# Optimization experiments

Hardware: AMD Instinct MI355X
Metric: run time of the kernel (lower is better)

The kernel has to match this reference:

```python
import jax, jax.numpy as jnp
import numpy as np
import math

# Static multi-level spatial layout (H, W) per level and flattened start offsets.
SHAPES = ((100, 100), (50, 50), (25, 25), (13, 13))
STARTS = (0, 10000, 12500, 13125)
LEN_IN = 13294
D_MODEL, N_LEVELS, N_HEADS, N_POINTS = 256, 4, 8, 4
D_HEAD = D_MODEL // N_HEADS
B, LQ = 2, 13294


def _offset_bias():
    # Replicates MSDeformAttn._reset_parameters radial grid init for sampling_offsets.bias
    thetas = np.arange(N_HEADS, dtype=np.float32) * (2.0 * math.pi / N_HEADS)
    grid = np.stack([np.cos(thetas), np.sin(thetas)], axis=-1)  # [nh, 2]
    grid = grid / np.abs(grid).max(axis=-1, keepdims=True)
    # [nh, nl, np, 2] with per-point radius (i+1)
    full = np.tile(grid[:, None, None, :], (1, N_LEVELS, N_POINTS, 1))
    full = full * np.arange(1, N_POINTS + 1, dtype=np.float32)[None, None, :, None]
    return full.reshape(-1)


def setup_inputs() -> dict:
    key = jax.random.key(0)
    ks = jax.random.split(key, 8)
    xavier = 1.0 / math.sqrt(D_MODEL)
    return {
        "query": jax.random.normal(ks[0], (B, LQ, D_MODEL), jnp.float32),
        "reference_points": jax.random.uniform(ks[1], (B, LQ, N_LEVELS, 2), jnp.float32),
        "input_flatten": jax.random.normal(ks[2], (B, LEN_IN, D_MODEL), jnp.float32),
        "input_spatial_shapes": jnp.array(SHAPES, jnp.int32),
        "input_level_start_index": jnp.array(STARTS, jnp.int32),
        "W_off": jax.random.normal(ks[3], (D_MODEL, N_HEADS * N_LEVELS * N_POINTS * 2), jnp.float32) * 0.01,
        "b_off": jnp.asarray(_offset_bias()),
        "W_attn": jax.random.normal(ks[4], (D_MODEL, N_HEADS * N_LEVELS * N_POINTS), jnp.float32) * 0.02,
        "b_attn": jnp.zeros((N_HEADS * N_LEVELS * N_POINTS,), jnp.float32),
        "W_val": jax.random.normal(ks[5], (D_MODEL, D_MODEL), jnp.float32) * xavier,
        "b_val": jnp.zeros((D_MODEL,), jnp.float32),
        "W_out": jax.random.normal(ks[6], (D_MODEL, D_MODEL), jnp.float32) * xavier,
        "b_out": jnp.zeros((D_MODEL,), jnp.float32),
    }


def reference(query, reference_points, input_flatten, input_spatial_shapes,
              input_level_start_index, W_off, b_off, W_attn, b_attn,
              W_val, b_val, W_out, b_out):
    Bq, Lq, _ = query.shape
    value = (input_flatten @ W_val + b_val).reshape(Bq, LEN_IN, N_HEADS, D_HEAD)

    off = (query @ W_off + b_off).reshape(Bq, Lq, N_HEADS, N_LEVELS, N_POINTS, 2)
    aw = (query @ W_attn + b_attn).reshape(Bq, Lq, N_HEADS, N_LEVELS * N_POINTS)
    aw = jax.nn.softmax(aw, axis=-1).reshape(Bq, Lq, N_HEADS, N_LEVELS, N_POINTS)

    # offset normalizer is (W, H) per level
    normalizer = jnp.array([[w, h] for (h, w) in SHAPES], query.dtype)  # [nl, 2]
    loc = reference_points[:, :, None, :, None, :] + off / normalizer[None, None, None, :, None, :]

    bi = jnp.arange(Bq)[:, None, None, None]
    hi = jnp.arange(N_HEADS)[None, None, :, None]
    out = jnp.zeros((Bq, Lq, N_HEADS, D_HEAD), query.dtype)

    # Per-level zero-padded bilinear sampling (math-equivalent to grid_sample
    # align_corners=False, padding_mode='zeros' on the padded max_H x max_W grid,
    # since the padded region is zero-filled).
    for lvl, (H, W) in enumerate(SHAPES):
        s = STARTS[lvl]
        vflat = value[:, s:s + H * W]  # [B, H*W, nh, dh]
        l = loc[:, :, :, lvl]          # [B, Lq, nh, P, 2] in normalized coords
        x = l[..., 0] * W - 0.5
        y = l[..., 1] * H - 0.5
        x0 = jnp.floor(x)
        y0 = jnp.floor(y)
        sampled = jnp.zeros((Bq, Lq, N_HEADS, N_POINTS, D_HEAD), query.dtype)
        for dx in (0, 1):
            for dy in (0, 1):
                xi = x0 + dx
                yi = y0 + dy
                wgt = (1.0 - jnp.abs(x - xi)) * (1.0 - jnp.abs(y - yi))
                valid = (xi >= 0) & (xi <= W - 1) & (yi >= 0) & (yi <= H - 1)
                idx = (jnp.clip(yi, 0, H - 1) * W + jnp.clip(xi, 0, W - 1)).astype(jnp.int32)
                v = vflat[bi, idx, hi]  # [B, Lq, nh, P, dh]
                sampled = sampled + v * (wgt * valid)[..., None]
        out = out + jnp.einsum('bqhpd,bqhp->bqhd', sampled, aw[:, :, :, lvl])

    out = out.reshape(Bq, Lq, D_MODEL)
    return out @ W_out + b_out
```

## Files before the change

### kernel.cpp

```cpp
#include <hip/hip_runtime.h>
#include <math.h>

#define BQ 2
#define LQ 13294
#define LEN_IN 13294
#define M_ROWS 26588

__device__ __constant__ int c_HW[4]    = {100, 50, 25, 13};
__device__ __constant__ int c_START[4] = {0, 10000, 12500, 13125};

typedef __attribute__((ext_vector_type(8))) short bf16x8;
typedef __attribute__((ext_vector_type(4))) float f32x4;
typedef __attribute__((ext_vector_type(2))) float f32x2;

__device__ inline unsigned short f2bf(float f) {
  union { float f; unsigned int u; } x; x.f = f;
  unsigned int u = x.u;
  return (unsigned short)((u + 0x7fffu + ((u >> 16) & 1u)) >> 16);
}
__device__ inline float h2f(unsigned short h) {
  _Float16 x; __builtin_memcpy(&x, &h, 2); return (float)x;
}
__device__ inline unsigned short f2h(float f) {
  _Float16 x = (_Float16)f; unsigned short u; __builtin_memcpy(&u, &x, 2); return u;
}

__device__ inline void gl_lds16(const void* g, void* l) {
  __builtin_amdgcn_global_load_lds(
      (const __attribute__((address_space(1))) unsigned int*)g,
      (__attribute__((address_space(3))) unsigned int*)l, 16, 0, 0);
}

__global__ __launch_bounds__(256) void prep_w(
    const float* __restrict__ W_off, const float* __restrict__ b_off,
    const float* __restrict__ W_attn, const float* __restrict__ b_attn,
    const float* __restrict__ W_val, const float* __restrict__ W_out,
    unsigned short* __restrict__ Wval_t, unsigned short* __restrict__ Woa_t,
    unsigned short* __restrict__ Wout_t, float* __restrict__ b_oa) {
  const int idx = blockIdx.x * 256 + threadIdx.x;
  const int SZ1 = 256 * 256;
  const int SZ2 = 384 * 256;
  if (idx < SZ1) {
    const int n = idx >> 8, k = idx & 255;
    Wval_t[idx] = f2bf(W_val[k * 256 + n]);
  } else if (idx < SZ1 + SZ2) {
    const int j = idx - SZ1;
    const int n = j >> 8, k = j & 255;
    const float v = (n < 256) ? W_off[k * 256 + n] : W_attn[k * 128 + (n - 256)];
    Woa_t[j] = f2bf(v);
  } else {
    const int j = idx - SZ1 - SZ2;
    const int n = j >> 8, k = j & 255;
    Wout_t[j] = f2bf(W_out[k * 256 + n]);
  }
  if (blockIdx.x == 0) b_oa[threadIdx.x] = b_off[threadIdx.x];
  if (blockIdx.x == 1 && threadIdx.x < 128)
    b_oa[256 + threadIdx.x] = b_attn[threadIdx.x];
}

__device__ inline void stage_W(const unsigned short* __restrict__ Wt,
                               int n0, int wv, int lane, unsigned short* Ws) {
#pragma unroll
  for (int it = 0; it < 16; ++it) {
    const int lin = wv * 1024 + it * 64 + lane;
    const int r = lin >> 5;
    const int p = lin & 31;
    const int c = p ^ (r & 7);
    gl_lds16(Wt + (size_t)(n0 + r) * 256 + c * 8,
             &Ws[(size_t)(wv * 1024 + it * 64) * 8]);
  }
}

template <int CT>
__device__ inline void kloop_epilogue(
    const bf16x8* a0f, const bf16x8* a1f, const unsigned short* Ws,
    const float* __restrict__ bias, void* __restrict__ Cp,
    int M, int N, int m0, int n0, int wv, int fr, int fq) {
  f32x4 acc[2][8];
#pragma unroll
  for (int mt = 0; mt < 2; ++mt)
#pragma unroll
    for (int n = 0; n < 8; ++n) acc[mt][n] = (f32x4){0.f, 0.f, 0.f, 0.f};

#pragma unroll
  for (int kk = 0; kk < 8; ++kk) {
#pragma unroll
    for (int n = 0; n < 8; ++n) {
      const int rn = n * 16 + fr;
      const bf16x8 b =
          *(const bf16x8*)&Ws[rn * 256 + (((kk * 4 + fq) ^ (rn & 7)) * 8)];
      acc[0][n] = __builtin_amdgcn_mfma_f32_16x16x32_bf16(b, a0f[kk], acc[0][n], 0, 0, 0);
      acc[1][n] = __builtin_amdgcn_mfma_f32_16x16x32_bf16(b, a1f[kk], acc[1][n], 0, 0, 0);
    }
  }

#pragma unroll
  for (int n = 0; n < 8; ++n) {
    const int nb = n0 + n * 16 + fq * 4;
    const float4 b4 = *(const float4*)&bias[nb];
#pragma unroll
    for (int mt = 0; mt < 2; ++mt) {
      const int m = m0 + wv * 32 + mt * 16 + fr;
      if (m >= M) continue;
      const float v0 = acc[mt][n][0] + b4.x;
      const float v1 = acc[mt][n][1] + b4.y;
      const float v2 = acc[mt][n][2] + b4.z;
      const float v3 = acc[mt][n][3] + b4.w;
      if (CT == 0) {
        *(float4*)&((float*)Cp)[(size_t)m * N + nb] = make_float4(v0, v1, v2, v3);
      } else if (CT == 1) {
        uint2 o;
        o.x = (unsigned int)f2bf(v0) | ((unsigned int)f2bf(v1) << 16);
        o.y = (unsigned int)f2bf(v2) | ((unsigned int)f2bf(v3) << 16);
        *(uint2*)&((unsigned short*)Cp)[(size_t)m * N + nb] = o;
      } else {
        uint2 o;
        o.x = (unsigned int)f2h(v0) | ((unsigned int)f2h(v1) << 16);
        o.y = (unsigned int)f2h(v2) | ((unsigned int)f2h(v3) << 16);
        *(uint2*)&((unsigned short*)Cp)[(size_t)m * N + nb] = o;
      }
    }
  }
}

template <int CT>
__device__ inline void gemm_stream_f32A(
    const float* __restrict__ A, const unsigned short* __restrict__ Wt,
    const float* __restrict__ bias, void* __restrict__ Cp,
    int M, int N, int m0, int n0, unsigned short* Ws) {
  const int tid = threadIdx.x;
  const int wv = tid >> 6;
  const int lane = tid & 63;
  const int fr = lane & 15;
  const int fq = lane >> 4;

  int mr0 = m0 + wv * 32 + fr;       if (mr0 > M - 1) mr0 = M - 1;
  int mr1 = m0 + wv * 32 + 16 + fr;  if (mr1 > M - 1) mr1 = M - 1;
  const float* a0 = A + (size_t)mr0 * 256 + fq * 8;
  const float* a1 = A + (size_t)mr1 * 256 + fq * 8;

  bf16x8 a0f[8], a1f[8];
#pragma unroll
  for (int kk = 0; kk < 8; ++kk) {
    const float4 x0 = *(const float4*)(a0 + kk * 32);
    const float4 x1 = *(const float4*)(a0 + kk * 32 + 4);
    const float4 y0 = *(const float4*)(a1 + kk * 32);
    const float4 y1 = *(const float4*)(a1 + kk * 32 + 4);
    ushort4 h0, h1;
    h0.x = f2bf(x0.x); h0.y = f2bf(x0.y); h0.z = f2bf(x0.z); h0.w = f2bf(x0.w);
    h1.x = f2bf(x1.x); h1.y = f2bf(x1.y); h1.z = f2bf(x1.z); h1.w = f2bf(x1.w);
    union { ushort4 h[2]; bf16x8 v; } u0; u0.h[0] = h0; u0.h[1] = h1;
    a0f[kk] = u0.v;
    h0.x = f2bf(y0.x); h0.y = f2bf(y0.y); h0.z = f2bf(y0.z); h0.w = f2bf(y0.w);
    h1.x = f2bf(y1.x); h1.y = f2bf(y1.y); h1.z = f2bf(y1.z); h1.w = f2bf(y1.w);
    union { ushort4 h[2]; bf16x8 v; } u1; u1.h[0] = h0; u1.h[1] = h1;
    a1f[kk] = u1.v;
  }

  stage_W(Wt, n0, wv, lane, Ws);
  __syncthreads();

  kloop_epilogue<CT>(a0f, a1f, Ws, bias, Cp, M, N, m0, n0, wv, fr, fq);
}

template <int CT>
__device__ inline void gemm_stream_bf16A(
    const unsigned short* __restrict__ A, const unsigned short* __restrict__ Wt,
    const float* __restrict__ bias, void* __restrict__ Cp,
    int M, int N, int m0, int n0, unsigned short* Ws) {
  const int tid = threadIdx.x;
  const int wv = tid >> 6;
  const int lane = tid & 63;
  const int fr = lane & 15;
  const int fq = lane >> 4;

  int mr0 = m0 + wv * 32 + fr;       if (mr0 > M - 1) mr0 = M - 1;
  int mr1 = m0 + wv * 32 + 16 + fr;  if (mr1 > M - 1) mr1 = M - 1;
  const unsigned short* a0 = A + (size_t)mr0 * 256 + fq * 8;
  const unsigned short* a1 = A + (size_t)mr1 * 256 + fq * 8;
  bf16x8 a0f[8], a1f[8];
#pragma unroll
  for (int kk = 0; kk < 8; ++kk) {
    a0f[kk] = *(const bf16x8*)(a0 + kk * 32);
    a1f[kk] = *(const bf16x8*)(a1 + kk * 32);
  }

  stage_W(Wt, n0, wv, lane, Ws);
  __syncthreads();

  kloop_epilogue<CT>(a0f, a1f, Ws, bias, Cp, M, N, m0, n0, wv, fr, fq);
}

__global__ __launch_bounds__(256) void gemm_vo(
    const float* __restrict__ inpf, const float* __restrict__ query,
    const unsigned short* __restrict__ Wval_t,
    const unsigned short* __restrict__ Woa_t,
    const float* __restrict__ b_val, const float* __restrict__ b_oa,
    void* __restrict__ v_buf, void* __restrict__ oa_buf) {
  __shared__ unsigned short Ws[128 * 256];
  const int m0 = blockIdx.x * 128;
  if (blockIdx.y < 2) {
    gemm_stream_f32A<1>(inpf, Wval_t, b_val, v_buf, M_ROWS, 256,
                        m0, blockIdx.y * 128, Ws);
  } else {
    gemm_stream_f32A<2>(query, Woa_t, b_oa, oa_buf, M_ROWS, 384,
                        m0, (blockIdx.y - 2) * 128, Ws);
  }
}

__global__ __launch_bounds__(256) void gemm_out(
    const unsigned short* __restrict__ mid,
    const unsigned short* __restrict__ Wout_t,
    const float* __restrict__ b_out, float* __restrict__ out) {
  __shared__ unsigned short Ws[128 * 256];
  gemm_stream_bf16A<0>(mid, Wout_t, b_out, out, M_ROWS, 256,
                       blockIdx.x * 128, blockIdx.y * 128, Ws);
}

__global__ __launch_bounds__(256) void sample_kernel(
    const float* __restrict__ refp,
    const unsigned short* __restrict__ oa,
    const unsigned short* __restrict__ value,
    unsigned int* __restrict__ mid) {
  const int tid = threadIdx.x;
  const int qi = tid >> 7;
  const int q = blockIdx.x * 2 + qi;
  const int b = (q >= LQ) ? 1 : 0;

  __shared__ float2 s_wo[2][4][136];

  {
    const int pid = tid & 127;
    const int h = pid >> 4;
    const int lp = pid & 15;
    const int l = lp >> 2;
    const int p = lp & 3;
    const int HW = c_HW[l];
    const float fW = (float)HW;

    const float logit = h2f(oa[(size_t)q * 384 + 256 + pid]);
    float mx = logit;
#pragma unroll
    for (int s = 1; s < 16; s <<= 1) mx = fmaxf(mx, __shfl_xor(mx, s, 16));
    const float e = expf(logit - mx);
    float sum = e;
#pragma unroll
    for (int s = 1; s < 16; s <<= 1) sum += __shfl_xor(sum, s, 16);
    const float a = e / sum;

    const unsigned int opk =
        *(const unsigned int*)&oa[(size_t)q * 384 + h * 32 + l * 8 + p * 2];
    const float ox = h2f((unsigned short)(opk & 0xffffu));
    const float oy = h2f((unsigned short)(opk >> 16));
    const float rx = refp[((size_t)q * 4 + l) * 2 + 0];
    const float ry = refp[((size_t)q * 4 + l) * 2 + 1];
    const float x = fmaf(rx, fW, ox - 0.5f);
    const float y = fmaf(ry, fW, oy - 0.5f);
    const float x0 = floorf(x);
    const float y0 = floorf(y);

#pragma unroll
    for (int t = 0; t < 4; ++t) {
      const int dx = t & 1;
      const int dy = t >> 1;
      const float xi = x0 + (float)dx;
      const float yi = y0 + (float)dy;
      const float wgt = (1.0f - fabsf(x - xi)) * (1.0f - fabsf(y - yi));
      const bool valid =
          (xi >= 0.f) && (xi <= fW - 1.f) && (yi >= 0.f) && (yi <= fW - 1.f);
      int xc = (int)xi; xc = xc < 0 ? 0 : (xc > HW - 1 ? HW - 1 : xc);
      int yc = (int)yi; yc = yc < 0 ? 0 : (yc > HW - 1 ? HW - 1 : yc);
      const int row = b * LEN_IN + c_START[l] + yc * HW + xc;
      float2 wo;
      wo.x = valid ? wgt * a : 0.f;
      wo.y = __int_as_float(row * 512 + h * 64);
      s_wo[qi][t][h * 17 + lp] = wo;
    }
  }
  __syncthreads();

  {
    const int g = tid & 127;
    const int h = g >> 4;
    const int dp = g & 15;
    const char* vbase = (const char*)value + dp * 4;
    f32x2 acc = {0.f, 0.f};
#pragma unroll 4
    for (int lp = 0; lp < 16; ++lp) {
      const int si = h * 17 + lp;
#pragma unroll
      for (int t = 0; t < 4; ++t) {
        const float2 f = s_wo[qi][t][si];
        const unsigned int v = *(const unsigned int*)(vbase + __float_as_int(f.y));
        f32x2 av = {__uint_as_float(v << 16), __uint_as_float(v & 0xffff0000u)};
        acc += f.x * av;
      }
    }
    mid[(size_t)q * 128 + h * 16 + dp] =
        (unsigned int)f2bf(acc.x) | ((unsigned int)f2bf(acc.y) << 16);
  }
}

extern "C" void kernel_launch(void* const* d_in, const int* in_sizes, int n_in,
                              void* d_out, int out_size, void* d_ws,
                              size_t ws_size, hipStream_t stream) {
  const float* query  = (const float*)d_in[0];
  const float* refp   = (const float*)d_in[1];
  const float* inpf   = (const float*)d_in[2];
  const float* W_off  = (const float*)d_in[5];
  const float* b_off  = (const float*)d_in[6];
  const float* W_attn = (const float*)d_in[7];
  const float* b_attn = (const float*)d_in[8];
  const float* W_val  = (const float*)d_in[9];
  const float* b_val  = (const float*)d_in[10];
  const float* W_out  = (const float*)d_in[11];
  const float* b_out  = (const float*)d_in[12];
  float* out = (float*)d_out;

  unsigned char* w = (unsigned char*)d_ws;
  unsigned short* Wval_t = (unsigned short*)w;  w += 256 * 256 * 2;
  unsigned short* Woa_t  = (unsigned short*)w;  w += 384 * 256 * 2;
  unsigned short* Wout_t = (unsigned short*)w;  w += 256 * 256 * 2;
  float*          b_oa   = (float*)w;           w += 384 * 4 + 64;
  unsigned short* v_buf  = (unsigned short*)w;  w += (size_t)M_ROWS * 256 * 2;
  unsigned short* oa_buf = (unsigned short*)w;  w += (size_t)M_ROWS * 384 * 2;
  unsigned int*   mid_buf = (unsigned int*)w;

  const dim3 blk(256);
  const int mg = (M_ROWS + 127) / 128;

  prep_w<<<dim3(896), blk, 0, stream>>>(W_off, b_off, W_attn, b_attn,
                                        W_val, W_out, Wval_t, Woa_t,
                                        Wout_t, b_oa);
  gemm_vo<<<dim3(mg, 5), blk, 0, stream>>>(inpf, query, Wval_t, Woa_t,
                                           b_val, b_oa, v_buf, oa_buf);
  sample_kernel<<<dim3(M_ROWS / 2), blk, 0, stream>>>(refp, oa_buf, v_buf,
                                                      mid_buf);
  gemm_out<<<dim3(mg, 2), blk, 0, stream>>>((const unsigned short*)mid_buf,
                                            Wout_t, b_out, out);
}
```

Baseline: 209.8 us.

## Load each A row block once and loop over all N tiles per block

The GEMM kernels change from a 2D grid, where each block loaded and converted its A rows for a single 128-column tile, to a 1D grid of 64-row blocks. Each block converts its A fragments once and then iterates over every N tile, restaging W into LDS each time. The aim is to stop re-reading and re-converting fp32 activations once per N tile. Packed bf16/f16 conversion intrinsics also replace the manual bit-twiddling rounding. The cost is less parallelism per block, serialized W staging with extra barriers, and half the M rows per wave per staged W tile.

```diff
diff --git a/kernel.cpp b/kernel.cpp
--- a/kernel.cpp
+++ b/kernel.cpp
@@ -1,4 +1,6 @@
 #include <hip/hip_runtime.h>
+#include <hip/hip_bf16.h>
+#include <hip/hip_fp16.h>
 #include <math.h>
 
 #define BQ 2
@@ -21,14 +23,30 @@
 __device__ inline float h2f(unsigned short h) {
   _Float16 x; __builtin_memcpy(&x, &h, 2); return (float)x;
 }
-__device__ inline unsigned short f2h(float f) {
-  _Float16 x = (_Float16)f; unsigned short u; __builtin_memcpy(&u, &x, 2); return u;
+__device__ inline unsigned int pk_bf16(float lo, float hi) {
+  __hip_bfloat162 h = __float22bfloat162_rn(make_float2(lo, hi));
+  unsigned int u; __builtin_memcpy(&u, &h, 4); return u;
+}
+__device__ inline unsigned int pk_f16(float lo, float hi) {
+  __half2 h = __float22half2_rn(make_float2(lo, hi));
+  unsigned int u; __builtin_memcpy(&u, &h, 4); return u;
 }
 
 __device__ inline void gl_lds16(const void* g, void* l) {
   __builtin_amdgcn_global_load_lds(
       (const __attribute__((address_space(1))) unsigned int*)g,
       (__attribute__((address_space(3))) unsigned int*)l, 16, 0, 0);
+}
+
+__device__ inline bf16x8 cvt8(const float* p) {
+  const float4 a = *(const float4*)p;
+  const float4 b = *(const float4*)(p + 4);
+  union { unsigned int u[4]; bf16x8 v; } r;
+  r.u[0] = pk_bf16(a.x, a.y);
+  r.u[1] = pk_bf16(a.z, a.w);
+  r.u[2] = pk_bf16(b.x, b.y);
+  r.u[3] = pk_bf16(b.z, b.w);
+  return r.v;
 }
 
 __global__ __launch_bounds__(256) void prep_w(
@@ -72,15 +90,19 @@
 }
 
 template <int CT>
-__device__ inline void kloop_epilogue(
-    const bf16x8* a0f, const bf16x8* a1f, const unsigned short* Ws,
-    const float* __restrict__ bias, void* __restrict__ Cp,
-    int M, int N, int m0, int n0, int wv, int fr, int fq) {
-  f32x4 acc[2][8];
-#pragma unroll
-  for (int mt = 0; mt < 2; ++mt)
-#pragma unroll
-    for (int n = 0; n < 8; ++n) acc[mt][n] = (f32x4){0.f, 0.f, 0.f, 0.f};
+__device__ inline void run_job(const bf16x8* af,
+                               const unsigned short* __restrict__ Wt,
+                               const float* __restrict__ bias,
+                               void* __restrict__ Cp, int N, int n0,
+                               int m, int wv, int lane, int fr, int fq,
+                               unsigned short* Ws) {
+  __syncthreads();
+  stage_W(Wt, n0, wv, lane, Ws);
+  __syncthreads();
+
+  f32x4 acc[8];
+#pragma unroll
+  for (int n = 0; n < 8; ++n) acc[n] = (f32x4){0.f, 0.f, 0.f, 0.f};
 
 #pragma unroll
   for (int kk = 0; kk < 8; ++kk) {
@@ -89,123 +111,60 @@
       const int rn = n * 16 + fr;
       const bf16x8 b =
           *(const bf16x8*)&Ws[rn * 256 + (((kk * 4 + fq) ^ (rn & 7)) * 8)];
-      acc[0][n] = __builtin_amdgcn_mfma_f32_16x16x32_bf16(b, a0f[kk], acc[0][n], 0, 0, 0);
-      acc[1][n] = __builtin_amdgcn_mfma_f32_16x16x32_bf16(b, a1f[kk], acc[1][n], 0, 0, 0);
+      acc[n] = __builtin_amdgcn_mfma_f32_16x16x32_bf16(b, af[kk], acc[n], 0, 0, 0);
     }
   }
 
-#pragma unroll
-  for (int n = 0; n < 8; ++n) {
-    const int nb = n0 + n * 16 + fq * 4;
-    const float4 b4 = *(const float4*)&bias[nb];
-#pragma unroll
-    for (int mt = 0; mt < 2; ++mt) {
-      const int m = m0 + wv * 32 + mt * 16 + fr;
-      if (m >= M) continue;
-      const float v0 = acc[mt][n][0] + b4.x;
-      const float v1 = acc[mt][n][1] + b4.y;
-      const float v2 = acc[mt][n][2] + b4.z;
-      const float v3 = acc[mt][n][3] + b4.w;
+  if (m < M_ROWS) {
+#pragma unroll
+    for (int n = 0; n < 8; ++n) {
+      const int nb = n0 + n * 16 + fq * 4;
+      const float4 b4 = *(const float4*)&bias[nb];
+      const float v0 = acc[n][0] + b4.x;
+      const float v1 = acc[n][1] + b4.y;
+      const float v2 = acc[n][2] + b4.z;
+      const float v3 = acc[n][3] + b4.w;
       if (CT == 0) {
         *(float4*)&((float*)Cp)[(size_t)m * N + nb] = make_float4(v0, v1, v2, v3);
       } else if (CT == 1) {
-        uint2 o;
-        o.x = (unsigned int)f2bf(v0) | ((unsigned int)f2bf(v1) << 16);
-        o.y = (unsigned int)f2bf(v2) | ((unsigned int)f2bf(v3) << 16);
+        uint2 o; o.x = pk_bf16(v0, v1); o.y = pk_bf16(v2, v3);
         *(uint2*)&((unsigned short*)Cp)[(size_t)m * N + nb] = o;
       } else {
-        uint2 o;
-        o.x = (unsigned int)f2h(v0) | ((unsigned int)f2h(v1) << 16);
-        o.y = (unsigned int)f2h(v2) | ((unsigned int)f2h(v3) << 16);
+        uint2 o; o.x = pk_f16(v0, v1); o.y = pk_f16(v2, v3);
         *(uint2*)&((unsigned short*)Cp)[(size_t)m * N + nb] = o;
       }
     }
   }
 }
 
-template <int CT>
-__device__ inline void gemm_stream_f32A(
-    const float* __restrict__ A, const unsigned short* __restrict__ Wt,
-    const float* __restrict__ bias, void* __restrict__ Cp,
-    int M, int N, int m0, int n0, unsigned short* Ws) {
-  const int tid = threadIdx.x;
-  const int wv = tid >> 6;
-  const int lane = tid & 63;
-  const int fr = lane & 15;
-  const int fq = lane >> 4;
-
-  int mr0 = m0 + wv * 32 + fr;       if (mr0 > M - 1) mr0 = M - 1;
-  int mr1 = m0 + wv * 32 + 16 + fr;  if (mr1 > M - 1) mr1 = M - 1;
-  const float* a0 = A + (size_t)mr0 * 256 + fq * 8;
-  const float* a1 = A + (size_t)mr1 * 256 + fq * 8;
-
-  bf16x8 a0f[8], a1f[8];
-#pragma unroll
-  for (int kk = 0; kk < 8; ++kk) {
-    const float4 x0 = *(const float4*)(a0 + kk * 32);
-    const float4 x1 = *(const float4*)(a0 + kk * 32 + 4);
-    const float4 y0 = *(const float4*)(a1 + kk * 32);
-    const float4 y1 = *(const float4*)(a1 + kk * 32 + 4);
-    ushort4 h0, h1;
-    h0.x = f2bf(x0.x); h0.y = f2bf(x0.y); h0.z = f2bf(x0.z); h0.w = f2bf(x0.w);
-    h1.x = f2bf(x1.x); h1.y = f2bf(x1.y); h1.z = f2bf(x1.z); h1.w = f2bf(x1.w);
-    union { ushort4 h[2]; bf16x8 v; } u0; u0.h[0] = h0; u0.h[1] = h1;
-    a0f[kk] = u0.v;
-    h0.x = f2bf(y0.x); h0.y = f2bf(y0.y); h0.z = f2bf(y0.z); h0.w = f2bf(y0.w);
-    h1.x = f2bf(y1.x); h1.y = f2bf(y1.y); h1.z = f2bf(y1.z); h1.w = f2bf(y1.w);
-    union { ushort4 h[2]; bf16x8 v; } u1; u1.h[0] = h0; u1.h[1] = h1;
-    a1f[kk] = u1.v;
-  }
-
-  stage_W(Wt, n0, wv, lane, Ws);
-  __syncthreads();
-
-  kloop_epilogue<CT>(a0f, a1f, Ws, bias, Cp, M, N, m0, n0, wv, fr, fq);
-}
-
-template <int CT>
-__device__ inline void gemm_stream_bf16A(
-    const unsigned short* __restrict__ A, const unsigned short* __restrict__ Wt,
-    const float* __restrict__ bias, void* __restrict__ Cp,
-    int M, int N, int m0, int n0, unsigned short* Ws) {
-  const int tid = threadIdx.x;
-  const int wv = tid >> 6;
-  const int lane = tid & 63;
-  const int fr = lane & 15;
-  const int fq = lane >> 4;
-
-  int mr0 = m0 + wv * 32 + fr;       if (mr0 > M - 1) mr0 = M - 1;
-  int mr1 = m0 + wv * 32 + 16 + fr;  if (mr1 > M - 1) mr1 = M - 1;
-  const unsigned short* a0 = A + (size_t)mr0 * 256 + fq * 8;
-  const unsigned short* a1 = A + (size_t)mr1 * 256 + fq * 8;
-  bf16x8 a0f[8], a1f[8];
-#pragma unroll
-  for (int kk = 0; kk < 8; ++kk) {
-    a0f[kk] = *(const bf16x8*)(a0 + kk * 32);
-    a1f[kk] = *(const bf16x8*)(a1 + kk * 32);
-  }
-
-  stage_W(Wt, n0, wv, lane, Ws);
-  __syncthreads();
-
-  kloop_epilogue<CT>(a0f, a1f, Ws, bias, Cp, M, N, m0, n0, wv, fr, fq);
-}
-
-__global__ __launch_bounds__(256) void gemm_vo(
+__global__ __launch_bounds__(256) void gemm_mlp(
     const float* __restrict__ inpf, const float* __restrict__ query,
     const unsigned short* __restrict__ Wval_t,
     const unsigned short* __restrict__ Woa_t,
     const float* __restrict__ b_val, const float* __restrict__ b_oa,
     void* __restrict__ v_buf, void* __restrict__ oa_buf) {
   __shared__ unsigned short Ws[128 * 256];
-  const int m0 = blockIdx.x * 128;
-  if (blockIdx.y < 2) {
-    gemm_stream_f32A<1>(inpf, Wval_t, b_val, v_buf, M_ROWS, 256,
-                        m0, blockIdx.y * 128, Ws);
-  } else {
-    gemm_stream_f32A<2>(query, Woa_t, b_oa, oa_buf, M_ROWS, 384,
-                        m0, (blockIdx.y - 2) * 128, Ws);
-  }
+  const int tid = threadIdx.x;
+  const int wv = tid >> 6;
+  const int lane = tid & 63;
+  const int fr = lane & 15;
+  const int fq = lane >> 4;
+  const int m = blockIdx.x * 64 + wv * 16 + fr;
+  const int mr = (m > M_ROWS - 1) ? (M_ROWS - 1) : m;
+
+  const float* ain = inpf + (size_t)mr * 256 + fq * 8;
+  const float* aq  = query + (size_t)mr * 256 + fq * 8;
+  bf16x8 fin[8], fqr[8];
+#pragma unroll
+  for (int kk = 0; kk < 8; ++kk) fin[kk] = cvt8(ain + kk * 32);
+#pragma unroll
+  for (int kk = 0; kk < 8; ++kk) fqr[kk] = cvt8(aq + kk * 32);
+
+  run_job<1>(fin, Wval_t, b_val, v_buf, 256, 0,   m, wv, lane, fr, fq, Ws);
+  run_job<1>(fin, Wval_t, b_val, v_buf, 256, 128, m, wv, lane, fr, fq, Ws);
+  run_job<2>(fqr, Woa_t, b_oa, oa_buf, 384, 0,   m, wv, lane, fr, fq, Ws);
+  run_job<2>(fqr, Woa_t, b_oa, oa_buf, 384, 128, m, wv, lane, fr, fq, Ws);
+  run_job<2>(fqr, Woa_t, b_oa, oa_buf, 384, 256, m, wv, lane, fr, fq, Ws);
 }
 
 __global__ __launch_bounds__(256) void gemm_out(
@@ -213,8 +172,21 @@
     const unsigned short* __restrict__ Wout_t,
     const float* __restrict__ b_out, float* __restrict__ out) {
   __shared__ unsigned short Ws[128 * 256];
-  gemm_stream_bf16A<0>(mid, Wout_t, b_out, out, M_ROWS, 256,
-                       blockIdx.x * 128, blockIdx.y * 128, Ws);
+  const int tid = threadIdx.x;
+  const int wv = tid >> 6;
+  const int lane = tid & 63;
+  const int fr = lane & 15;
+  const int fq = lane >> 4;
+  const int m = blockIdx.x * 64 + wv * 16 + fr;
+  const int mr = (m > M_ROWS - 1) ? (M_ROWS - 1) : m;
+
+  const unsigned short* a = mid + (size_t)mr * 256 + fq * 8;
+  bf16x8 af[8];
+#pragma unroll
+  for (int kk = 0; kk < 8; ++kk) af[kk] = *(const bf16x8*)(a + kk * 32);
+
+  run_job<0>(af, Wout_t, b_out, out, 256, 0,   m, wv, lane, fr, fq, Ws);
+  run_job<0>(af, Wout_t, b_out, out, 256, 128, m, wv, lane, fr, fq, Ws);
 }
 
 __global__ __launch_bounds__(256) void sample_kernel(
@@ -296,8 +268,7 @@
         acc += f.x * av;
       }
     }
-    mid[(size_t)q * 128 + h * 16 + dp] =
-        (unsigned int)f2bf(acc.x) | ((unsigned int)f2bf(acc.y) << 16);
+    mid[(size_t)q * 128 + h * 16 + dp] = pk_bf16(acc.x, acc.y);
   }
 }
 
@@ -327,15 +298,15 @@
   unsigned int*   mid_buf = (unsigned int*)w;
 
   const dim3 blk(256);
-  const int mg = (M_ROWS + 127) / 128;
+  const int mg64 = (M_ROWS + 63) / 64;
 
   prep_w<<<dim3(896), blk, 0, stream>>>(W_off, b_off, W_attn, b_attn,
                                         W_val, W_out, Wval_t, Woa_t,
                                         Wout_t, b_oa);
-  gemm_vo<<<dim3(mg, 5), blk, 0, stream>>>(inpf, query, Wval_t, Woa_t,
+  gemm_mlp<<<dim3(mg64), blk, 0, stream>>>(inpf, query, Wval_t, Woa_t,
                                            b_val, b_oa, v_buf, oa_buf);
   sample_kernel<<<dim3(M_ROWS / 2), blk, 0, stream>>>(refp, oa_buf, v_buf,
                                                       mid_buf);
-  gemm_out<<<dim3(mg, 2), blk, 0, stream>>>((const unsigned short*)mid_buf,
-                                            Wout_t, b_out, out);
-}
+  gemm_out<<<dim3(mg64), blk, 0, stream>>>((const unsigned short*)mid_buf,
+                                           Wout_t, b_out, out);
+}
```

After: 215.3 us. 1.03x slower.
